# Optimization experiments

Hardware: AMD Instinct MI355X
Metric: run time of the kernel (lower is better)

The kernel has to match this reference:

```python
import jax, jax.numpy as jnp
import numpy as np

B, L, H = 1024, 256, 128
NUM_TEAMS, NUM_VENUES, NUM_RESULTS = 1000, 3, 3
OUT_IN = 4 * H + 2 + 3  # past_repr (4H+2) concat stats (3)


def setup_inputs() -> dict:
    key = jax.random.key(0)
    ks = jax.random.split(key, 16)
    return {
        "team_embed": jax.random.normal(ks[0], (NUM_TEAMS, H), jnp.float32) * 0.02,
        "venue_embed": jax.random.normal(ks[1], (NUM_VENUES, H), jnp.float32) * 0.02,
        "result_embed": jax.random.normal(ks[2], (NUM_RESULTS, H), jnp.float32) * 0.02,
        "W_out": jax.random.normal(ks[3], (OUT_IN, NUM_RESULTS), jnp.float32) * 0.02,
        "b_out": jnp.zeros((NUM_RESULTS,), jnp.float32),
        "goals_for": jax.random.uniform(ks[4], (B, L), jnp.float32) * 5.0,
        "goals_against": jax.random.uniform(ks[5], (B, L), jnp.float32) * 5.0,
        "stats": jax.random.uniform(ks[6], (B, 3), jnp.float32),
        "venue": jax.random.randint(ks[7], (B, L), 0, NUM_VENUES),
        "team": jax.random.randint(ks[8], (B, L), 0, NUM_TEAMS),
        "opponent": jax.random.randint(ks[9], (B, L), 0, NUM_TEAMS),
        "result": jax.random.randint(ks[10], (B, L), 0, NUM_RESULTS),
        "next_venue": jax.random.randint(ks[11], (B,), 0, NUM_VENUES),
        "next_team": jax.random.randint(ks[12], (B,), 0, NUM_TEAMS),
        "next_opponent": jax.random.randint(ks[13], (B,), 0, NUM_TEAMS),
    }


def reference(team_embed, venue_embed, result_embed, W_out, b_out,
              goals_for, goals_against, stats,
              venue, team, opponent, result,
              next_venue, next_team, next_opponent):
    h = team_embed.shape[1]
    # (B, L, 4H+2): embedding gathers + goal scalars concatenated
    past_seq = jnp.concatenate([
        venue_embed[venue], team_embed[team], team_embed[opponent],
        result_embed[result], goals_for[..., None], goals_against[..., None],
    ], axis=-1)
    # (B, 3H): next-match condition vector
    next_cond = jnp.concatenate([
        venue_embed[next_venue], team_embed[next_team], team_embed[next_opponent],
    ], axis=-1)
    scale = jnp.asarray(3 * h, past_seq.dtype) ** 0.5
    scores = jnp.einsum('bld,bd->bl', past_seq[..., : 3 * h], next_cond) / scale
    attn = jax.nn.softmax(scores, axis=1)                 # over L
    past_repr = jnp.einsum('bl,bld->bd', attn, past_seq)  # (B, 4H+2)
    logits = jnp.concatenate([past_repr, stats], axis=-1) @ W_out + b_out
    return logits
```

## Files before the change

### kernel.cpp

```cpp
#include <hip/hip_runtime.h>

#define L_ 256
#define H_ 128

#define KSCALE 0.07362222315f

__global__ __launch_bounds__(256) void fused_match_kernel(
    const float* __restrict__ team_embed,
    const float* __restrict__ venue_embed,
    const float* __restrict__ result_embed,
    const float* __restrict__ W_out,
    const float* __restrict__ b_out,
    const float* __restrict__ goals_for,
    const float* __restrict__ goals_against,
    const float* __restrict__ stats,
    const int* __restrict__ venue,
    const int* __restrict__ team,
    const int* __restrict__ opponent,
    const int* __restrict__ result,
    const int* __restrict__ next_venue,
    const int* __restrict__ next_team,
    const int* __restrict__ next_opponent,
    float* __restrict__ out)
{
    const int b    = blockIdx.x;
    const int t    = threadIdx.x;
    const int lane = t & 63;
    const int wid  = t >> 6;
    const int half = lane >> 5;
    const int c    = lane & 31;

    __shared__ float  nc[384];
    __shared__ int    s_team[L_];
    __shared__ int    s_opp[L_];
    __shared__ float  s_score[L_];
    __shared__ float  s_dv[L_];
    __shared__ float  s_dotv[3];
    __shared__ float  s_m[8];
    __shared__ float4 s_accT[8][32];
    __shared__ float4 s_accO[8][32];
    __shared__ float  s_reds[4];
    __shared__ float  s_redw[4][8];
    __shared__ float  s_w[8];
    __shared__ float  s_pr[517];

    const int base = b * L_;
    const int my_venue  = venue[base + t];
    const int my_result = result[base + t];
    const float my_gf   = goals_for[base + t];
    const float my_ga   = goals_against[base + t];
    s_team[t] = team[base + t];
    s_opp[t]  = opponent[base + t];

    const int nv  = next_venue[b];
    const int ntm = next_team[b];
    const int nop = next_opponent[b];
    if (t < 128) {
        nc[t]       = venue_embed[nv * H_ + t];
        nc[128 + t] = team_embed[ntm * H_ + t];
    } else {
        nc[128 + t] = team_embed[nop * H_ + (t - 128)];
    }
    __syncthreads();

    if (wid < 3) {
        float a = venue_embed[wid * H_ + lane]      * nc[lane]
                + venue_embed[wid * H_ + 64 + lane] * nc[64 + lane];
        #pragma unroll
        for (int off = 32; off > 0; off >>= 1) a += __shfl_down(a, off);
        if (lane == 0) s_dotv[wid] = a;
    }
    __syncthreads();
    s_dv[t] = s_dotv[my_venue];
    __syncthreads();

    const float4 nct_c = ((const float4*)(nc + 128))[c];
    const float4 nco_c = ((const float4*)(nc + 256))[c];
    const int    lb    = wid * 64 + half * 32;
    float4 accT = make_float4(0.f, 0.f, 0.f, 0.f);
    float4 accO = make_float4(0.f, 0.f, 0.f, 0.f);
    float  mrun = -1e30f;
    #pragma unroll 4
    for (int i = 0; i < 32; ++i) {
        const int l = lb + i;
        const float4 vT = ((const float4*)team_embed)[s_team[l] * 32 + c];
        const float4 vO = ((const float4*)team_embed)[s_opp[l]  * 32 + c];
        float p = vT.x * nct_c.x + vT.y * nct_c.y + vT.z * nct_c.z + vT.w * nct_c.w
                + vO.x * nco_c.x + vO.y * nco_c.y + vO.z * nco_c.z + vO.w * nco_c.w;
        #pragma unroll
        for (int k = 16; k > 0; k >>= 1) p += __shfl_xor(p, k);
        const float kk = (p + s_dv[l]) * KSCALE;
        if ((lane & 31) == 0) s_score[l] = kk;
        if (kk > mrun) {
            const float alpha = exp2f(mrun - kk);
            accT.x *= alpha; accT.y *= alpha; accT.z *= alpha; accT.w *= alpha;
            accO.x *= alpha; accO.y *= alpha; accO.z *= alpha; accO.w *= alpha;
            mrun = kk;
        }
        const float e = exp2f(kk - mrun);
        accT.x += e * vT.x; accT.y += e * vT.y; accT.z += e * vT.z; accT.w += e * vT.w;
        accO.x += e * vO.x; accO.y += e * vO.y; accO.z += e * vO.z; accO.w += e * vO.w;
    }
    {
        const int hw = wid * 2 + half;
        if ((lane & 31) == 0) s_m[hw] = mrun;
        s_accT[hw][c] = accT;
        s_accO[hw][c] = accO;
    }
    __syncthreads();

    float M = s_m[0];
    #pragma unroll
    for (int j = 1; j < 8; ++j) M = fmaxf(M, s_m[j]);

    const float e = exp2f(s_score[t] - M);
    float vals[8];
    vals[0] = (my_venue  == 0) ? e : 0.f;
    vals[1] = (my_venue  == 1) ? e : 0.f;
    vals[2] = (my_venue  == 2) ? e : 0.f;
    vals[3] = (my_result == 0) ? e : 0.f;
    vals[4] = (my_result == 1) ? e : 0.f;
    vals[5] = (my_result == 2) ? e : 0.f;
    vals[6] = e * my_gf;
    vals[7] = e * my_ga;
    float sum = e;
    #pragma unroll
    for (int off = 32; off > 0; off >>= 1) {
        sum += __shfl_down(sum, off);
        #pragma unroll
        for (int k = 0; k < 8; ++k) vals[k] += __shfl_down(vals[k], off);
    }
    if (lane == 0) {
        s_reds[wid] = sum;
        #pragma unroll
        for (int k = 0; k < 8; ++k) s_redw[wid][k] = vals[k];
    }
    __syncthreads();
    const float Z    = s_reds[0] + s_reds[1] + s_reds[2] + s_reds[3];
    const float invZ = 1.f / Z;
    if (t < 8)
        s_w[t] = (s_redw[0][t] + s_redw[1][t] + s_redw[2][t] + s_redw[3][t]) * invZ;
    __syncthreads();

    if (t < 64) {
        const int seg = t >> 5;
        const int cc  = t & 31;
        float4 a = make_float4(0.f, 0.f, 0.f, 0.f);
        #pragma unroll
        for (int h = 0; h < 8; ++h) {
            const float sc  = exp2f(s_m[h] - M);
            const float4 v  = seg ? s_accO[h][cc] : s_accT[h][cc];
            a.x += sc * v.x; a.y += sc * v.y; a.z += sc * v.z; a.w += sc * v.w;
        }
        const int d = 128 + seg * 128 + cc * 4;
        s_pr[d + 0] = a.x * invZ;
        s_pr[d + 1] = a.y * invZ;
        s_pr[d + 2] = a.z * invZ;
        s_pr[d + 3] = a.w * invZ;
        if (t < 2) s_pr[512 + t] = s_w[6 + t];
        if (t >= 2 && t < 5) s_pr[512 + t] = stats[b * 3 + t - 2];
    } else if (t < 192) {
        const int j = t - 64;
        s_pr[j] = s_w[0] * venue_embed[j] + s_w[1] * venue_embed[H_ + j]
                + s_w[2] * venue_embed[2 * H_ + j];
    } else {
        const int j = t - 192;
        s_pr[384 + j] = s_w[3] * result_embed[j]      + s_w[4] * result_embed[H_ + j]
                      + s_w[5] * result_embed[2 * H_ + j];
        s_pr[448 + j] = s_w[3] * result_embed[64 + j] + s_w[4] * result_embed[H_ + 64 + j]
                      + s_w[5] * result_embed[2 * H_ + 64 + j];
    }
    __syncthreads();

    if (wid < 3) {
        float acc = 0.f;
        for (int d = lane; d < 517; d += 64) acc += s_pr[d] * W_out[d * 3 + wid];
        #pragma unroll
        for (int off = 32; off > 0; off >>= 1) acc += __shfl_down(acc, off);
        if (lane == 0) out[b * 3 + wid] = acc + b_out[wid];
    }
}

extern "C" void kernel_launch(void* const* d_in, const int* in_sizes, int n_in,
                              void* d_out, int out_size, void* d_ws, size_t ws_size,
                              hipStream_t stream) {
    const float* team_embed    = (const float*)d_in[0];
    const float* venue_embed   = (const float*)d_in[1];
    const float* result_embed  = (const float*)d_in[2];
    const float* W_out         = (const float*)d_in[3];
    const float* b_out         = (const float*)d_in[4];
    const float* goals_for     = (const float*)d_in[5];
    const float* goals_against = (const float*)d_in[6];
    const float* stats         = (const float*)d_in[7];
    const int* venue           = (const int*)d_in[8];
    const int* team            = (const int*)d_in[9];
    const int* opponent        = (const int*)d_in[10];
    const int* result          = (const int*)d_in[11];
    const int* next_venue      = (const int*)d_in[12];
    const int* next_team       = (const int*)d_in[13];
    const int* next_opponent   = (const int*)d_in[14];
    float* out = (float*)d_out;

    const int B = in_sizes[12];
    fused_match_kernel<<<B, 256, 0, stream>>>(
        team_embed, venue_embed, result_embed, W_out, b_out,
        goals_for, goals_against, stats,
        venue, team, opponent, result,
        next_venue, next_team, next_opponent, out);
}
```

Before: 108.2 us.

## Split attention over sequence halves into partial and finalize kernels

Each batch row's 256-step attention is split across two blocks of 128 steps each. Their unnormalized partial sums go to workspace, and a second kernel combines them and computes the output projection. The online-max rescaling is dropped in favor of plain exp2 without max subtraction, which assumes scores stay small enough not to overflow. This doubles block count to raise parallelism and trims per-step work, at the cost of a second launch, a workspace round trip, and the loss of the max-stabilized softmax.

```diff
diff --git a/kernel.cpp b/kernel.cpp
--- a/kernel.cpp
+++ b/kernel.cpp
@@ -5,15 +5,13 @@
 
 #define KSCALE 0.07362222315f
 
-__global__ __launch_bounds__(256) void fused_match_kernel(
+#define REC_STRIDE 272
+
+__global__ __launch_bounds__(256, 8) void partial_kernel(
     const float* __restrict__ team_embed,
     const float* __restrict__ venue_embed,
-    const float* __restrict__ result_embed,
-    const float* __restrict__ W_out,
-    const float* __restrict__ b_out,
     const float* __restrict__ goals_for,
     const float* __restrict__ goals_against,
-    const float* __restrict__ stats,
     const int* __restrict__ venue,
     const int* __restrict__ team,
     const int* __restrict__ opponent,
@@ -21,155 +19,156 @@
     const int* __restrict__ next_venue,
     const int* __restrict__ next_team,
     const int* __restrict__ next_opponent,
+    float* __restrict__ ws)
+{
+    const int b    = blockIdx.x >> 1;
+    const int j    = blockIdx.x & 1;
+    const int t    = threadIdx.x;
+    const int lane = t & 63;
+    const int wid  = t >> 6;
+    const int half = lane >> 5;
+    const int c    = lane & 31;
+
+    __shared__ float  nc[384];
+    __shared__ int    s_team[128];
+    __shared__ int    s_opp[128];
+    __shared__ int    s_vi[128];
+    __shared__ int    s_ri[128];
+    __shared__ float  s_gf[128];
+    __shared__ float  s_ga[128];
+    __shared__ float  s_e[128];
+    __shared__ float  s_dotv[3];
+    __shared__ float4 s_accT[8][32];
+    __shared__ float4 s_accO[8][32];
+    __shared__ float  s_red[2][9];
+
+    const int base = b * L_ + j * 128;
+    if (t < 128) {
+        s_team[t] = team[base + t];
+        s_opp[t]  = opponent[base + t];
+        s_vi[t]   = venue[base + t];
+        s_ri[t]   = result[base + t];
+        s_gf[t]   = goals_for[base + t];
+        s_ga[t]   = goals_against[base + t];
+    }
+    const int nv  = next_venue[b];
+    const int ntm = next_team[b];
+    const int nop = next_opponent[b];
+    if (t < 128) {
+        nc[t]       = venue_embed[nv * H_ + t];
+        nc[128 + t] = team_embed[ntm * H_ + t];
+    } else {
+        nc[128 + t] = team_embed[nop * H_ + (t - 128)];
+    }
+    __syncthreads();
+
+    if (wid < 3) {
+        float a = venue_embed[wid * H_ + lane]      * nc[lane]
+                + venue_embed[wid * H_ + 64 + lane] * nc[64 + lane];
+        #pragma unroll
+        for (int off = 32; off > 0; off >>= 1) a += __shfl_down(a, off);
+        if (lane == 0) s_dotv[wid] = a;
+    }
+    __syncthreads();
+
+    const float4 nct_c = ((const float4*)(nc + 128))[c];
+    const float4 nco_c = ((const float4*)(nc + 256))[c];
+    const int hw = wid * 2 + half;
+    const int lb = hw * 16;
+    float4 accT = make_float4(0.f, 0.f, 0.f, 0.f);
+    float4 accO = make_float4(0.f, 0.f, 0.f, 0.f);
+    #pragma unroll 4
+    for (int i = 0; i < 16; ++i) {
+        const int l = lb + i;
+        const float4 vT = ((const float4*)team_embed)[s_team[l] * 32 + c];
+        const float4 vO = ((const float4*)team_embed)[s_opp[l]  * 32 + c];
+        float p = vT.x * nct_c.x + vT.y * nct_c.y + vT.z * nct_c.z + vT.w * nct_c.w
+                + vO.x * nco_c.x + vO.y * nco_c.y + vO.z * nco_c.z + vO.w * nco_c.w;
+        #pragma unroll
+        for (int k = 16; k > 0; k >>= 1) p += __shfl_xor(p, k);
+        const float e = exp2f((p + s_dotv[s_vi[l]]) * KSCALE);
+        if ((lane & 31) == 0) s_e[l] = e;
+        accT.x += e * vT.x; accT.y += e * vT.y; accT.z += e * vT.z; accT.w += e * vT.w;
+        accO.x += e * vO.x; accO.y += e * vO.y; accO.z += e * vO.z; accO.w += e * vO.w;
+    }
+    s_accT[hw][c] = accT;
+    s_accO[hw][c] = accO;
+    __syncthreads();
+
+    if (t < 128) {
+        const float e = s_e[t];
+        const int vi = s_vi[t], ri = s_ri[t];
+        float vals[9];
+        vals[0] = e;
+        vals[1] = (vi == 0) ? e : 0.f;
+        vals[2] = (vi == 1) ? e : 0.f;
+        vals[3] = (vi == 2) ? e : 0.f;
+        vals[4] = (ri == 0) ? e : 0.f;
+        vals[5] = (ri == 1) ? e : 0.f;
+        vals[6] = (ri == 2) ? e : 0.f;
+        vals[7] = e * s_gf[t];
+        vals[8] = e * s_ga[t];
+        #pragma unroll
+        for (int off = 32; off > 0; off >>= 1) {
+            #pragma unroll
+            for (int k = 0; k < 9; ++k) vals[k] += __shfl_down(vals[k], off);
+        }
+        if (lane == 0) {
+            #pragma unroll
+            for (int k = 0; k < 9; ++k) s_red[wid][k] = vals[k];
+        }
+    }
+    __syncthreads();
+
+    float* rec = ws + (size_t)blockIdx.x * REC_STRIDE;
+    if (t < 9) rec[256 + t] = s_red[0][t] + s_red[1][t];
+    if (t < 64) {
+        const int seg = t >> 5, cc = t & 31;
+        float4 a = make_float4(0.f, 0.f, 0.f, 0.f);
+        #pragma unroll
+        for (int h = 0; h < 8; ++h) {
+            const float4 v = seg ? s_accO[h][cc] : s_accT[h][cc];
+            a.x += v.x; a.y += v.y; a.z += v.z; a.w += v.w;
+        }
+        *((float4*)(rec + seg * 128 + cc * 4)) = a;
+    }
+}
+
+__global__ __launch_bounds__(256) void finalize_kernel(
+    const float* __restrict__ venue_embed,
+    const float* __restrict__ result_embed,
+    const float* __restrict__ W_out,
+    const float* __restrict__ b_out,
+    const float* __restrict__ stats,
+    const float* __restrict__ ws,
     float* __restrict__ out)
 {
     const int b    = blockIdx.x;
     const int t    = threadIdx.x;
     const int lane = t & 63;
     const int wid  = t >> 6;
-    const int half = lane >> 5;
-    const int c    = lane & 31;
-
-    __shared__ float  nc[384];
-    __shared__ int    s_team[L_];
-    __shared__ int    s_opp[L_];
-    __shared__ float  s_score[L_];
-    __shared__ float  s_dv[L_];
-    __shared__ float  s_dotv[3];
-    __shared__ float  s_m[8];
-    __shared__ float4 s_accT[8][32];
-    __shared__ float4 s_accO[8][32];
-    __shared__ float  s_reds[4];
-    __shared__ float  s_redw[4][8];
-    __shared__ float  s_w[8];
-    __shared__ float  s_pr[517];
-
-    const int base = b * L_;
-    const int my_venue  = venue[base + t];
-    const int my_result = result[base + t];
-    const float my_gf   = goals_for[base + t];
-    const float my_ga   = goals_against[base + t];
-    s_team[t] = team[base + t];
-    s_opp[t]  = opponent[base + t];
-
-    const int nv  = next_venue[b];
-    const int ntm = next_team[b];
-    const int nop = next_opponent[b];
-    if (t < 128) {
-        nc[t]       = venue_embed[nv * H_ + t];
-        nc[128 + t] = team_embed[ntm * H_ + t];
+
+    __shared__ float s_pr[517];
+    __shared__ float s_w[8];
+
+    const float* r0 = ws + (size_t)(b * 2) * REC_STRIDE;
+    const float* r1 = r0 + REC_STRIDE;
+    const float invZ = 1.f / (r0[256] + r1[256]);
+
+    s_pr[128 + t] = (r0[t] + r1[t]) * invZ;
+    if (t < 8) s_w[t] = (r0[257 + t] + r1[257 + t]) * invZ;
+    __syncthreads();
+
+    if (t < 128) {
+        s_pr[t] = s_w[0] * venue_embed[t] + s_w[1] * venue_embed[H_ + t]
+                + s_w[2] * venue_embed[2 * H_ + t];
     } else {
-        nc[128 + t] = team_embed[nop * H_ + (t - 128)];
-    }
-    __syncthreads();
-
-    if (wid < 3) {
-        float a = venue_embed[wid * H_ + lane]      * nc[lane]
-                + venue_embed[wid * H_ + 64 + lane] * nc[64 + lane];
-        #pragma unroll
-        for (int off = 32; off > 0; off >>= 1) a += __shfl_down(a, off);
-        if (lane == 0) s_dotv[wid] = a;
-    }
-    __syncthreads();
-    s_dv[t] = s_dotv[my_venue];
-    __syncthreads();
-
-    const float4 nct_c = ((const float4*)(nc + 128))[c];
-    const float4 nco_c = ((const float4*)(nc + 256))[c];
-    const int    lb    = wid * 64 + half * 32;
-    float4 accT = make_float4(0.f, 0.f, 0.f, 0.f);
-    float4 accO = make_float4(0.f, 0.f, 0.f, 0.f);
-    float  mrun = -1e30f;
-    #pragma unroll 4
-    for (int i = 0; i < 32; ++i) {
-        const int l = lb + i;
-        const float4 vT = ((const float4*)team_embed)[s_team[l] * 32 + c];
-        const float4 vO = ((const float4*)team_embed)[s_opp[l]  * 32 + c];
-        float p = vT.x * nct_c.x + vT.y * nct_c.y + vT.z * nct_c.z + vT.w * nct_c.w
-                + vO.x * nco_c.x + vO.y * nco_c.y + vO.z * nco_c.z + vO.w * nco_c.w;
-        #pragma unroll
-        for (int k = 16; k > 0; k >>= 1) p += __shfl_xor(p, k);
-        const float kk = (p + s_dv[l]) * KSCALE;
-        if ((lane & 31) == 0) s_score[l] = kk;
-        if (kk > mrun) {
-            const float alpha = exp2f(mrun - kk);
-            accT.x *= alpha; accT.y *= alpha; accT.z *= alpha; accT.w *= alpha;
-            accO.x *= alpha; accO.y *= alpha; accO.z *= alpha; accO.w *= alpha;
-            mrun = kk;
-        }
-        const float e = exp2f(kk - mrun);
-        accT.x += e * vT.x; accT.y += e * vT.y; accT.z += e * vT.z; accT.w += e * vT.w;
-        accO.x += e * vO.x; accO.y += e * vO.y; accO.z += e * vO.z; accO.w += e * vO.w;
-    }
-    {
-        const int hw = wid * 2 + half;
-        if ((lane & 31) == 0) s_m[hw] = mrun;
-        s_accT[hw][c] = accT;
-        s_accO[hw][c] = accO;
-    }
-    __syncthreads();
-
-    float M = s_m[0];
-    #pragma unroll
-    for (int j = 1; j < 8; ++j) M = fmaxf(M, s_m[j]);
-
-    const float e = exp2f(s_score[t] - M);
-    float vals[8];
-    vals[0] = (my_venue  == 0) ? e : 0.f;
-    vals[1] = (my_venue  == 1) ? e : 0.f;
-    vals[2] = (my_venue  == 2) ? e : 0.f;
-    vals[3] = (my_result == 0) ? e : 0.f;
-    vals[4] = (my_result == 1) ? e : 0.f;
-    vals[5] = (my_result == 2) ? e : 0.f;
-    vals[6] = e * my_gf;
-    vals[7] = e * my_ga;
-    float sum = e;
-    #pragma unroll
-    for (int off = 32; off > 0; off >>= 1) {
-        sum += __shfl_down(sum, off);
-        #pragma unroll
-        for (int k = 0; k < 8; ++k) vals[k] += __shfl_down(vals[k], off);
-    }
-    if (lane == 0) {
-        s_reds[wid] = sum;
-        #pragma unroll
-        for (int k = 0; k < 8; ++k) s_redw[wid][k] = vals[k];
-    }
-    __syncthreads();
-    const float Z    = s_reds[0] + s_reds[1] + s_reds[2] + s_reds[3];
-    const float invZ = 1.f / Z;
-    if (t < 8)
-        s_w[t] = (s_redw[0][t] + s_redw[1][t] + s_redw[2][t] + s_redw[3][t]) * invZ;
-    __syncthreads();
-
-    if (t < 64) {
-        const int seg = t >> 5;
-        const int cc  = t & 31;
-        float4 a = make_float4(0.f, 0.f, 0.f, 0.f);
-        #pragma unroll
-        for (int h = 0; h < 8; ++h) {
-            const float sc  = exp2f(s_m[h] - M);
-            const float4 v  = seg ? s_accO[h][cc] : s_accT[h][cc];
-            a.x += sc * v.x; a.y += sc * v.y; a.z += sc * v.z; a.w += sc * v.w;
-        }
-        const int d = 128 + seg * 128 + cc * 4;
-        s_pr[d + 0] = a.x * invZ;
-        s_pr[d + 1] = a.y * invZ;
-        s_pr[d + 2] = a.z * invZ;
-        s_pr[d + 3] = a.w * invZ;
-        if (t < 2) s_pr[512 + t] = s_w[6 + t];
-        if (t >= 2 && t < 5) s_pr[512 + t] = stats[b * 3 + t - 2];
-    } else if (t < 192) {
-        const int j = t - 64;
-        s_pr[j] = s_w[0] * venue_embed[j] + s_w[1] * venue_embed[H_ + j]
-                + s_w[2] * venue_embed[2 * H_ + j];
-    } else {
-        const int j = t - 192;
-        s_pr[384 + j] = s_w[3] * result_embed[j]      + s_w[4] * result_embed[H_ + j]
-                      + s_w[5] * result_embed[2 * H_ + j];
-        s_pr[448 + j] = s_w[3] * result_embed[64 + j] + s_w[4] * result_embed[H_ + 64 + j]
-                      + s_w[5] * result_embed[2 * H_ + 64 + j];
-    }
+        const int jj = t - 128;
+        s_pr[384 + jj] = s_w[3] * result_embed[jj] + s_w[4] * result_embed[H_ + jj]
+                       + s_w[5] * result_embed[2 * H_ + jj];
+    }
+    if (t == 0) { s_pr[512] = s_w[6]; s_pr[513] = s_w[7]; }
+    if (t < 3)  s_pr[514 + t] = stats[b * 3 + t];
     __syncthreads();
 
     if (wid < 3) {
@@ -200,11 +199,13 @@
     const int* next_team       = (const int*)d_in[13];
     const int* next_opponent   = (const int*)d_in[14];
     float* out = (float*)d_out;
+    float* ws  = (float*)d_ws;
 
     const int B = in_sizes[12];
-    fused_match_kernel<<<B, 256, 0, stream>>>(
-        team_embed, venue_embed, result_embed, W_out, b_out,
-        goals_for, goals_against, stats,
+    partial_kernel<<<B * 2, 256, 0, stream>>>(
+        team_embed, venue_embed, goals_for, goals_against,
         venue, team, opponent, result,
-        next_venue, next_team, next_opponent, out);
+        next_venue, next_team, next_opponent, ws);
+    finalize_kernel<<<B, 256, 0, stream>>>(
+        venue_embed, result_embed, W_out, b_out, stats, ws, out);
 }
```

Result: slower. 112.5 us (+4.0%).
